# Kernel optimization log

Measured on AMD Instinct MI355X. Metric: run time of the kernel, lower is better.

The kernel has to match this reference:

```python
import jax, jax.numpy as jnp
import numpy as np

N_NODE = 100_000
N_EDGE = 2_000_000
IN_DIM = 64
OUT_DIM = 64
ATTN_DIM = 32
N_REL = 200   # rela_embed has 2*N_REL+1 = 401 rows
N_ENT = 50_000
BATCH = 8


def setup_inputs() -> dict:
    key = jax.random.key(0)
    ks = jax.random.split(key, 16)
    # edges columns: 0=r_idx (query index in batch), 2=rel, 4=sub, 5=obj; cols 1,3 unused
    r_idx = jax.random.randint(ks[0], (N_EDGE,), 0, BATCH, dtype=jnp.int32)
    rel = jax.random.randint(ks[1], (N_EDGE,), 0, 2 * N_REL + 1, dtype=jnp.int32)
    sub = jax.random.randint(ks[2], (N_EDGE,), 0, N_NODE, dtype=jnp.int32)
    obj = jax.random.randint(ks[3], (N_EDGE,), 0, N_NODE, dtype=jnp.int32)
    pad = jnp.zeros((N_EDGE,), jnp.int32)
    edges = jnp.stack([r_idx, pad, rel, pad, sub, obj], axis=1)
    nodes = jnp.stack(
        [jax.random.randint(ks[4], (N_NODE,), 0, BATCH, dtype=jnp.int32),
         jax.random.randint(ks[5], (N_NODE,), 0, N_ENT, dtype=jnp.int32)], axis=1)
    s = 0.05
    return {
        "q_sub": jax.random.randint(ks[6], (BATCH,), 0, N_ENT, dtype=jnp.int32),
        "q_rel": jax.random.randint(ks[7], (BATCH,), 0, 2 * N_REL + 1, dtype=jnp.int32),
        "hidden": jax.random.normal(ks[8], (N_NODE, IN_DIM), jnp.float32),
        "edges": edges,
        "nodes": nodes,
        "old_nodes_new_idx": jnp.arange(N_NODE // 2, dtype=jnp.int32),
        "batchsize": BATCH,
        "rela_embed": jax.random.normal(ks[9], (2 * N_REL + 1, IN_DIM), jnp.float32) * s,
        "Ws": jax.random.normal(ks[10], (ATTN_DIM, IN_DIM), jnp.float32) * s,
        "Wr": jax.random.normal(ks[11], (ATTN_DIM, IN_DIM), jnp.float32) * s,
        "Wqr": jax.random.normal(ks[12], (ATTN_DIM, IN_DIM), jnp.float32) * s,
        "bqr": jax.random.normal(ks[13], (ATTN_DIM,), jnp.float32) * s,
        "w_alpha_w": jax.random.normal(ks[14], (1, ATTN_DIM), jnp.float32) * s,
        "w_alpha_b": jnp.zeros((1,), jnp.float32),
        "Wh": jax.random.normal(ks[15], (OUT_DIM, IN_DIM), jnp.float32) * s,
    }


def reference(q_sub, q_rel, hidden, edges, nodes, old_nodes_new_idx, batchsize,
              rela_embed, Ws, Wr, Wqr, bqr, w_alpha_w, w_alpha_b, Wh):
    sub = edges[:, 4]
    rel = edges[:, 2]
    obj = edges[:, 5]
    r_idx = edges[:, 0]
    n_node = hidden.shape[0]

    hs = hidden[sub]                      # [E, in_dim] gather
    hr = rela_embed[rel]                  # [E, in_dim] gather
    h_qr = rela_embed[q_rel][r_idx]       # [E, in_dim] gather of per-query rel embed

    # attention: sigmoid(w_alpha(relu(Ws hs + Wr hr + Wqr h_qr + bqr)))
    attn = jax.nn.relu(hs @ Ws.T + hr @ Wr.T + h_qr @ Wqr.T + bqr)  # [E, attn_dim]
    alpha = jax.nn.sigmoid(attn @ w_alpha_w.T + w_alpha_b)           # [E, 1]

    message = alpha * (hs + hr)           # [E, in_dim]
    message_agg = jax.ops.segment_sum(message, obj, num_segments=n_node)  # [n_node, in_dim]
    hidden_new = message_agg @ Wh.T       # act is identity (default)
    return hidden_new
```

## Files before the change

kernel.cpp:

```cpp
#include <hip/hip_runtime.h>
#include <hip/hip_bf16.h>
#include <hip/hip_fp16.h>


typedef __attribute__((ext_vector_type(8))) short bf16x8;
typedef __attribute__((ext_vector_type(4))) float f32x4;
typedef __attribute__((ext_vector_type(2))) float f32x2;

__device__ inline unsigned short f2bf(float x) {
    unsigned u = __float_as_uint(x);
    u += 0x7FFF + ((u >> 16) & 1);
    return (unsigned short)(u >> 16);
}
__device__ inline float bf2f(unsigned short b) {
    return __uint_as_float(((unsigned)b) << 16);
}
__device__ inline __half2 u2h2(unsigned u) {
    return __builtin_bit_cast(__half2, u);
}

__device__ inline bf16x8 pack8(float4 a, float4 b) {
    bf16x8 r;
    r[0] = (short)f2bf(a.x); r[1] = (short)f2bf(a.y);
    r[2] = (short)f2bf(a.z); r[3] = (short)f2bf(a.w);
    r[4] = (short)f2bf(b.x); r[5] = (short)f2bf(b.y);
    r[6] = (short)f2bf(b.z); r[7] = (short)f2bf(b.w);
    return r;
}

template<int NT, bool F16>
__global__ void proj_mfma2_kernel(const float* __restrict__ X1, int n1,
                                  const float* __restrict__ X2, int n2,
                                  const float* __restrict__ W,
                                  unsigned short* __restrict__ out1,
                                  unsigned short* __restrict__ out2) {
    int nb1 = (n1 + 63) / 64;
    const float* X; unsigned short* out; int nrows, mblk;
    if ((int)blockIdx.x < nb1) { X = X1; out = out1; nrows = n1; mblk = blockIdx.x; }
    else                        { X = X2; out = out2; nrows = n2; mblk = blockIdx.x - nb1; }

    int lane = threadIdx.x & 63;
    int wv   = threadIdx.x >> 6;
    int m0   = (mblk * 4 + wv) * 16;
    if (m0 >= nrows) return;
    int lr = lane & 15;
    int lk = lane >> 4;

    bf16x8 bfr[NT][2];
#pragma unroll
    for (int nt = 0; nt < NT; ++nt)
#pragma unroll
        for (int ks = 0; ks < 2; ++ks) {
            const float* wp = W + (size_t)(nt * 16 + lr) * 64 + ks * 32 + lk * 8;
            float4 w0 = *(const float4*)wp;
            float4 w1 = *(const float4*)(wp + 4);
            bfr[nt][ks] = pack8(w0, w1);
        }

    int row = m0 + lr;
    if (row >= nrows) row = nrows - 1;
    const float* xp = X + (size_t)row * 64 + lk * 8;
    float4 x0 = *(const float4*)xp;
    float4 x1 = *(const float4*)(xp + 4);
    float4 x2 = *(const float4*)(xp + 32);
    float4 x3 = *(const float4*)(xp + 36);
    bf16x8 a0 = pack8(x0, x1);
    bf16x8 a1 = pack8(x2, x3);

    f32x4 acc[NT];
#pragma unroll
    for (int nt = 0; nt < NT; ++nt) {
        acc[nt] = (f32x4){0.f, 0.f, 0.f, 0.f};
        acc[nt] = __builtin_amdgcn_mfma_f32_16x16x32_bf16(a0, bfr[nt][0], acc[nt], 0, 0, 0);
        acc[nt] = __builtin_amdgcn_mfma_f32_16x16x32_bf16(a1, bfr[nt][1], acc[nt], 0, 0, 0);
    }

#pragma unroll
    for (int nt = 0; nt < NT; ++nt)
#pragma unroll
        for (int r = 0; r < 4; ++r) {
            int ro = m0 + lk * 4 + r;
            if (ro < nrows) {
                unsigned short bits;
                if (F16) {
                    __half h = __float2half(acc[nt][r]);
                    bits = __builtin_bit_cast(unsigned short, h);
                } else {
                    bits = f2bf(acc[nt][r]);
                }
                out[(size_t)ro * (NT * 16) + nt * 16 + lr] = bits;
            }
        }
}

__global__ void qproj_bf16_kernel(const int* __restrict__ q_rel, const float* __restrict__ rela,
                                  const float* __restrict__ Wqr, const float* __restrict__ bqr,
                                  unsigned* __restrict__ Qb, int batch) {
    int tid = threadIdx.x;
    int b = tid >> 5, k = tid & 31;
    if (b >= batch) return;
    int qr = q_rel[b];
    const float* x = rela + (size_t)qr * 64;
    const float* w = Wqr + (size_t)k * 64;
    float acc = bqr[k];
    for (int d = 0; d < 64; ++d) acc += w[d] * x[d];
    float other = __shfl_xor(acc, 1, 64);
    if ((k & 1) == 0) {
        unsigned lo = f2bf(acc), hi = f2bf(other);
        Qb[b * 16 + (k >> 1)] = lo | (hi << 16);
    }
}

__global__ void pack_hist_kernel(const int4* __restrict__ edges4, int2* __restrict__ pk2,
                                 int* __restrict__ hmat, int n_edge, int NB) {
    __shared__ int hist[512];
    int tid = threadIdx.x, blk = blockIdx.x;
    hist[tid] = 0;
    hist[tid + 256] = 0;
    __syncthreads();
    int unit0 = blk * 2048;
#pragma unroll
    for (int k = 0; k < 8; ++k) {
        int u = unit0 + k * 256 + tid;
        int base = u * 4;
        if (base >= n_edge) break;
        if (base + 4 <= n_edge) {
            const int4* p = edges4 + (size_t)u * 6;
            int4 v0 = p[0], v1 = p[1], v2 = p[2], v3 = p[3], v4 = p[4], v5 = p[5];
            atomicAdd(&hist[v1.y >> 8], 1);
            atomicAdd(&hist[v2.w >> 8], 1);
            atomicAdd(&hist[v4.y >> 8], 1);
            atomicAdd(&hist[v5.w >> 8], 1);
            int4 o0, o1;
            o0.x = v1.x | (v0.z << 17) | (v0.x << 26); o0.y = v1.y;
            o0.z = v2.z | (v2.x << 17) | (v1.z << 26); o0.w = v2.w;
            o1.x = v4.x | (v3.z << 17) | (v3.x << 26); o1.y = v4.y;
            o1.z = v5.z | (v5.x << 17) | (v4.z << 26); o1.w = v5.w;
            int4* q = (int4*)pk2 + (size_t)u * 2;
            q[0] = o0;
            q[1] = o1;
        } else {
            const int* ei = (const int*)edges4;
            for (int e = base; e < n_edge; ++e) {
                const int* ep = ei + (size_t)e * 6;
                int ridx = ep[0], rel = ep[2], sub = ep[4], obj = ep[5];
                atomicAdd(&hist[obj >> 8], 1);
                pk2[e] = make_int2(sub | (rel << 17) | (ridx << 26), obj);
            }
        }
    }
    __syncthreads();
    hmat[tid * NB + blk] = hist[tid];
    hmat[(tid + 256) * NB + blk] = hist[tid + 256];
}

#define SCAN_CHUNK 1024

__global__ void scan_partial_kernel(const int* __restrict__ counts, int* __restrict__ bsum,
                                    int N) {
    __shared__ int s[256];
    int base = blockIdx.x * SCAN_CHUNK;
    int tid = threadIdx.x;
    int sum = 0;
#pragma unroll
    for (int k = 0; k < 4; ++k) {
        int idx = base + k * 256 + tid;
        if (idx < N) sum += counts[idx];
    }
    s[tid] = sum;
    __syncthreads();
    for (int off = 128; off > 0; off >>= 1) {
        if (tid < off) s[tid] += s[tid + off];
        __syncthreads();
    }
    if (tid == 0) bsum[blockIdx.x] = s[0];
}

__global__ void scan_bsum_kernel(int* __restrict__ bsum, int* __restrict__ offs, int B, int N) {
    __shared__ int s[1024];
    int tid = threadIdx.x;
    int v = (tid < B) ? bsum[tid] : 0;
    s[tid] = v;
    __syncthreads();
    for (int off = 1; off < 1024; off <<= 1) {
        int t = (tid >= off) ? s[tid - off] : 0;
        __syncthreads();
        s[tid] += t;
        __syncthreads();
    }
    if (tid < B) bsum[tid] = s[tid] - v;
    if (tid == 0) offs[N] = s[1023];
}

__global__ void scan_final_kernel(const int* __restrict__ counts, const int* __restrict__ bsum,
                                  int* __restrict__ offs, int N) {
    __shared__ int s[256];
    int base = blockIdx.x * SCAN_CHUNK;
    int tid = threadIdx.x;
    int v[4];
    int sum = 0;
#pragma unroll
    for (int k = 0; k < 4; ++k) {
        int idx = base + tid * 4 + k;
        v[k] = (idx < N) ? counts[idx] : 0;
        sum += v[k];
    }
    s[tid] = sum;
    __syncthreads();
    for (int off = 1; off < 256; off <<= 1) {
        int t = (tid >= off) ? s[tid - off] : 0;
        __syncthreads();
        s[tid] += t;
        __syncthreads();
    }
    int run = bsum[blockIdx.x] + s[tid] - sum;
#pragma unroll
    for (int k = 0; k < 4; ++k) {
        int idx = base + tid * 4 + k;
        if (idx < N) offs[idx] = run;
        run += v[k];
    }
}

__global__ void scatter1_kernel(const int2* __restrict__ pk2, const int* __restrict__ hscan,
                                int2* __restrict__ outrec, int n_edge, int NB) {
    __shared__ int cur[512];
    int tid = threadIdx.x, blk = blockIdx.x;
    cur[tid] = hscan[tid * NB + blk];
    cur[tid + 256] = hscan[(tid + 256) * NB + blk];
    __syncthreads();
    int unit0 = blk * 2048;
#pragma unroll
    for (int k = 0; k < 8; ++k) {
        int u = unit0 + k * 256 + tid;
        int base = u * 4;
        if (base >= n_edge) break;
        if (base + 4 <= n_edge) {
            const int4* q = (const int4*)pk2 + (size_t)u * 2;
            int4 a = q[0], b = q[1];
            int p0 = atomicAdd(&cur[(a.y >> 8) & 0x1FF], 1);
            int p1 = atomicAdd(&cur[(a.w >> 8) & 0x1FF], 1);
            int p2 = atomicAdd(&cur[(b.y >> 8) & 0x1FF], 1);
            int p3 = atomicAdd(&cur[(b.w >> 8) & 0x1FF], 1);
            outrec[p0] = make_int2(a.x, a.y);
            outrec[p1] = make_int2(a.z, a.w);
            outrec[p2] = make_int2(b.x, b.y);
            outrec[p3] = make_int2(b.z, b.w);
        } else {
            for (int e = base; e < n_edge; ++e) {
                int2 r = pk2[e];
                int p = atomicAdd(&cur[(r.y >> 8) & 0x1FF], 1);
                outrec[p] = r;
            }
        }
    }
}

#define BS_CAP 8192
__global__ __launch_bounds__(512) void bucket_sort_kernel(const int2* __restrict__ in,
                                                          const int* __restrict__ hscan,
                                                          int* __restrict__ hdrS,
                                                          int* __restrict__ offs,
                                                          int NB, int n_node) {
    __shared__ int hist[256];
    __shared__ int sbase[256];
    __shared__ int cur[256];
    __shared__ int2 st[BS_CAP];
    int b = blockIdx.x, tid = threadIdx.x;
    int start = hscan[b * NB];
    int end   = hscan[(b + 1) * NB];
    int size  = end - start;
    if (tid < 256) hist[tid] = 0;
    __syncthreads();
    bool inlds = (size <= BS_CAP);
    if (inlds) {
        for (int i = tid; i < size; i += 512) {
            int2 v = in[start + i];
            st[i] = v;
            atomicAdd(&hist[v.y & 255], 1);
        }
    } else {
        for (int i = tid; i < size; i += 512) {
            int2 v = in[start + i];
            atomicAdd(&hist[v.y & 255], 1);
        }
    }
    __syncthreads();
    int h = 0;
    if (tid < 256) { h = hist[tid]; sbase[tid] = h; }
    __syncthreads();
    for (int off = 1; off < 256; off <<= 1) {
        int t = (tid >= off && tid < 256) ? sbase[tid - off] : 0;
        __syncthreads();
        if (tid < 256) sbase[tid] += t;
        __syncthreads();
    }
    if (tid < 256) {
        int ebase = sbase[tid] - h;
        cur[tid] = ebase;
        int obj = (b << 8) | tid;
        if (obj <= n_node) offs[obj] = start + ebase;
    }
    __syncthreads();
    if (inlds) {
        for (int i = tid; i < size; i += 512) {
            int2 r = st[i];
            int p = atomicAdd(&cur[r.y & 255], 1);
            hdrS[start + p] = r.x;
        }
    } else {
        for (int i = tid; i < size; i += 512) {
            int2 r = in[start + i];
            int p = atomicAdd(&cur[r.y & 255], 1);
            hdrS[start + p] = r.x;
        }
    }
}

__device__ inline float edot(unsigned sv, unsigned rv, unsigned qv, float2 w) {
    float a0 = fmaxf(bf2f((unsigned short)sv) + bf2f((unsigned short)rv)
                     + bf2f((unsigned short)qv), 0.f);
    float a1 = fmaxf(bf2f((unsigned short)(sv >> 16)) + bf2f((unsigned short)(rv >> 16))
                     + bf2f((unsigned short)(qv >> 16)), 0.f);
    return a0 * w.x + a1 * w.y;
}

__global__ void alpha_kernel(const int* __restrict__ hdrS,
                             const unsigned* __restrict__ Sb,
                             const unsigned* __restrict__ Rb,
                             const unsigned* __restrict__ Qb,
                             const float2* __restrict__ w2,
                             const float* __restrict__ w_alpha_b,
                             float* __restrict__ af,
                             int n_edge) {
    int tid = threadIdx.x;
    int lane = tid & 15;
    int e0 = (blockIdx.x * 16 + (tid >> 4)) * 4;
    if (e0 >= n_edge) return;
    int4 h4 = *(const int4*)(hdrS + e0);
    int h0 = h4.x, h1 = h4.y, h2 = h4.z, h3 = h4.w;
    float2 w = w2[lane];
    unsigned sv0 = Sb[(size_t)(h0 & 0x1FFFF) * 16 + lane];
    unsigned sv1 = Sb[(size_t)(h1 & 0x1FFFF) * 16 + lane];
    unsigned sv2 = Sb[(size_t)(h2 & 0x1FFFF) * 16 + lane];
    unsigned sv3 = Sb[(size_t)(h3 & 0x1FFFF) * 16 + lane];
    unsigned rv0 = Rb[(size_t)((h0 >> 17) & 0x1FF) * 16 + lane];
    unsigned rv1 = Rb[(size_t)((h1 >> 17) & 0x1FF) * 16 + lane];
    unsigned rv2 = Rb[(size_t)((h2 >> 17) & 0x1FF) * 16 + lane];
    unsigned rv3 = Rb[(size_t)((h3 >> 17) & 0x1FF) * 16 + lane];
    unsigned qv0 = Qb[((h0 >> 26) & 7) * 16 + lane];
    unsigned qv1 = Qb[((h1 >> 26) & 7) * 16 + lane];
    unsigned qv2 = Qb[((h2 >> 26) & 7) * 16 + lane];
    unsigned qv3 = Qb[((h3 >> 26) & 7) * 16 + lane];
    float p0 = edot(sv0, rv0, qv0, w);
    float p1 = edot(sv1, rv1, qv1, w);
    float p2 = edot(sv2, rv2, qv2, w);
    float p3 = edot(sv3, rv3, qv3, w);
#pragma unroll
    for (int off = 8; off > 0; off >>= 1) {
        p0 += __shfl_xor(p0, off, 16);
        p1 += __shfl_xor(p1, off, 16);
        p2 += __shfl_xor(p2, off, 16);
        p3 += __shfl_xor(p3, off, 16);
    }
    if (lane < 4 && e0 + lane < n_edge) {
        float p = p0;
        if (lane == 1) p = p1;
        if (lane == 2) p = p2;
        if (lane == 3) p = p3;
        float alpha = 1.f / (1.f + __expf(-(p + w_alpha_b[0])));
        af[e0 + lane] = alpha;
    }
}

__global__ void reduce_kernel(const int* __restrict__ hdrS, const float* __restrict__ af,
                              const int* __restrict__ offs,
                              const uint2* __restrict__ Hw2,
                              const uint2* __restrict__ Rw2,
                              float4* __restrict__ out4, int n_node) {
    int lane = threadIdx.x & 63;
    int node = blockIdx.x * 4 + (threadIdx.x >> 6);
    if (node >= n_node) return;
    int g = lane >> 4;
    int t = lane & 15;
    int start = offs[node], end = offs[node + 1];
    __half2 acc0 = __float2half2_rn(0.f);
    __half2 acc1 = __float2half2_rn(0.f);

    for (int i = start; i < end; i += 64) {
        int m = end - i;
        if (m > 64) m = 64;
        float a = 0.f;
        int pk = 0;
        if (lane < m) {
            a  = __builtin_nontemporal_load(&af[i + lane]);
            pk = __builtin_nontemporal_load(&hdrS[i + lane]);
        }
        int nj = (m + 3) >> 2;

        __half2 A0, A1, A2, A3;
        uint2 H0, H1, H2, H3, R0, R1, R2, R3;

#define RD_ISSUE(S, J) do {                                                   \
        int src_ = 4 * (J) + g;                                               \
        bool ok_ = (src_ < m);                                                \
        int s_ = ok_ ? src_ : 0;                                              \
        float a_ = __shfl(a, s_, 64);                                         \
        int p_ = __shfl(pk, s_, 64);                                          \
        A##S = __float2half2_rn(ok_ ? a_ : 0.f);                              \
        int sub_ = p_ & 0x1FFFF, rel_ = (p_ >> 17) & 0x1FF;                   \
        H##S = Hw2[(size_t)sub_ * 16 + t];                                    \
        R##S = Rw2[(size_t)rel_ * 16 + t];                                    \
    } while (0)

#define RD_CONSUME(S) do {                                                    \
        acc0 = __hfma2(A##S, __hadd2(u2h2(H##S.x), u2h2(R##S.x)), acc0);      \
        acc1 = __hfma2(A##S, __hadd2(u2h2(H##S.y), u2h2(R##S.y)), acc1);      \
    } while (0)

        RD_ISSUE(0, 0);
        RD_ISSUE(1, 1);
        RD_ISSUE(2, 2);
        RD_ISSUE(3, 3);
        for (int j = 0; j < nj; j += 4) {
            RD_CONSUME(0); RD_ISSUE(0, j + 4);
            RD_CONSUME(1); RD_ISSUE(1, j + 5);
            RD_CONSUME(2); RD_ISSUE(2, j + 6);
            RD_CONSUME(3); RD_ISSUE(3, j + 7);
        }
#undef RD_ISSUE
#undef RD_CONSUME
    }
    float2 f0 = __half22float2(acc0);
    float2 f1 = __half22float2(acc1);
    f32x4 acc = (f32x4){f0.x, f0.y, f1.x, f1.y};
#pragma unroll
    for (int off = 16; off <= 32; off <<= 1) {
        acc.x += __shfl_xor(acc.x, off, 64);
        acc.y += __shfl_xor(acc.y, off, 64);
        acc.z += __shfl_xor(acc.z, off, 64);
        acc.w += __shfl_xor(acc.w, off, 64);
    }
    if (g == 0)
        __builtin_nontemporal_store(acc, (f32x4*)&out4[(size_t)node * 16 + t]);
}

extern "C" void kernel_launch(void* const* d_in, const int* in_sizes, int n_in,
                              void* d_out, int out_size, void* d_ws, size_t ws_size,
                              hipStream_t stream) {
    const int*   q_rel     = (const int*)d_in[1];
    const float* hidden    = (const float*)d_in[2];
    const int*   edges     = (const int*)d_in[3];
    const float* rela      = (const float*)d_in[7];
    const float* Ws        = (const float*)d_in[8];
    const float* Wr        = (const float*)d_in[9];
    const float* Wqr       = (const float*)d_in[10];
    const float* bqr       = (const float*)d_in[11];
    const float* w_alpha_w = (const float*)d_in[12];
    const float* w_alpha_b = (const float*)d_in[13];
    const float* Wh        = (const float*)d_in[14];

    int n_node = in_sizes[2] / 64;
    int n_edge = in_sizes[3] / 6;
    int n_rel  = in_sizes[7] / 64;
    int batch  = in_sizes[1];

    int NB = (n_edge + 8191) / 8192;
    int N2 = NB * 512;
    int n_sblk2 = (N2 + SCAN_CHUNK - 1) / SCAN_CHUNK;

    unsigned* Sb   = (unsigned*)d_ws;
    unsigned* Rb   = Sb + (size_t)n_node * 16;
    unsigned* Qb   = Rb + (size_t)n_rel * 16;
    int*   offs    = (int*)(Qb + (size_t)batch * 16);
    int*   bsum    = offs + n_node + 1;
    int*   hmat    = bsum + 1024;
    int*   hscan   = hmat + N2;
    size_t rec_off = (size_t)(hscan + N2 + 1 - (int*)d_ws);
    rec_off = (rec_off + 3) & ~(size_t)3;
    int2*  regP    = (int2*)((int*)d_ws + rec_off);
    int2*  regQ    = regP + n_edge;
    int*   hdrS    = (int*)regP;
    float* af      = (float*)(hdrS + n_edge);
    unsigned short* Hw = (unsigned short*)regQ;
    unsigned short* Rw = Hw + (size_t)n_node * 64;

    {
        int nb = (n_node + 63) / 64 + (n_rel + 63) / 64;
        proj_mfma2_kernel<2, false><<<nb, 256, 0, stream>>>(
            hidden, n_node, rela, n_rel, Ws, (unsigned short*)Sb, (unsigned short*)Rb);
    }
    qproj_bf16_kernel<<<1, 256, 0, stream>>>(q_rel, rela, Wqr, bqr, Qb, batch);

    pack_hist_kernel<<<NB, 256, 0, stream>>>((const int4*)edges, regP, hmat, n_edge, NB);

    scan_partial_kernel<<<n_sblk2, 256, 0, stream>>>(hmat, bsum, N2);
    scan_bsum_kernel<<<1, 1024, 0, stream>>>(bsum, hscan, n_sblk2, N2);
    scan_final_kernel<<<n_sblk2, 256, 0, stream>>>(hmat, bsum, hscan, N2);

    scatter1_kernel<<<NB, 256, 0, stream>>>(regP, hscan, regQ, n_edge, NB);
    bucket_sort_kernel<<<512, 512, 0, stream>>>(regQ, hscan, hdrS, offs, NB, n_node);

    alpha_kernel<<<(n_edge + 63) / 64, 256, 0, stream>>>(
        hdrS, Sb, Rb, Qb, (const float2*)w_alpha_w, w_alpha_b, af, n_edge);

    {
        int nb = (n_node + 63) / 64 + (n_rel + 63) / 64;
        proj_mfma2_kernel<4, true><<<nb, 256, 0, stream>>>(
            hidden, n_node, rela, n_rel, Wh, Hw, Rw);
    }

    reduce_kernel<<<(n_node + 3) / 4, 256, 0, stream>>>(
        hdrS, af, offs, (const uint2*)Hw, (const uint2*)Rw, (float4*)d_out, n_node);
}
```

Measured before the change: 304.1 us.

## Stage radix scatter through LDS to coalesce bucket writes

The first-pass radix scatter now loads each block's 8192 records, builds a local histogram, and scans it. It then sorts the records by bucket in shared memory before writing them out. Writes to global memory become contiguous runs per bucket instead of random 8-byte stores. The cost is 64KB+ of LDS per block, which lowers occupancy, plus extra syncs and a 512-step scan per block.

```diff
diff --git a/kernel.cpp b/kernel.cpp
--- a/kernel.cpp
+++ b/kernel.cpp
@@ -222,37 +222,58 @@
     }
 }
 
-__global__ void scatter1_kernel(const int2* __restrict__ pk2, const int* __restrict__ hscan,
-                                int2* __restrict__ outrec, int n_edge, int NB) {
-    __shared__ int cur[512];
+__global__ __launch_bounds__(512) void scatter1_kernel(const int2* __restrict__ pk2,
+                                                       const int* __restrict__ hscan,
+                                                       int2* __restrict__ outrec,
+                                                       int n_edge, int NB) {
+    __shared__ int lhist[512];
+    __shared__ int lincl[512];
+    __shared__ int lcur[512];
+    __shared__ int gbase[512];
+    __shared__ int2 st[8192];
     int tid = threadIdx.x, blk = blockIdx.x;
-    cur[tid] = hscan[tid * NB + blk];
-    cur[tid + 256] = hscan[(tid + 256) * NB + blk];
-    __syncthreads();
-    int unit0 = blk * 2048;
-#pragma unroll
-    for (int k = 0; k < 8; ++k) {
-        int u = unit0 + k * 256 + tid;
-        int base = u * 4;
-        if (base >= n_edge) break;
-        if (base + 4 <= n_edge) {
-            const int4* q = (const int4*)pk2 + (size_t)u * 2;
-            int4 a = q[0], b = q[1];
-            int p0 = atomicAdd(&cur[(a.y >> 8) & 0x1FF], 1);
-            int p1 = atomicAdd(&cur[(a.w >> 8) & 0x1FF], 1);
-            int p2 = atomicAdd(&cur[(b.y >> 8) & 0x1FF], 1);
-            int p3 = atomicAdd(&cur[(b.w >> 8) & 0x1FF], 1);
-            outrec[p0] = make_int2(a.x, a.y);
-            outrec[p1] = make_int2(a.z, a.w);
-            outrec[p2] = make_int2(b.x, b.y);
-            outrec[p3] = make_int2(b.z, b.w);
-        } else {
-            for (int e = base; e < n_edge; ++e) {
-                int2 r = pk2[e];
-                int p = atomicAdd(&cur[(r.y >> 8) & 0x1FF], 1);
-                outrec[p] = r;
-            }
-        }
+    int start_e = blk * 8192;
+    int cnt = n_edge - start_e;
+    if (cnt > 8192) cnt = 8192;
+    lhist[tid] = 0;
+    gbase[tid] = hscan[tid * NB + blk];
+    __syncthreads();
+    int2 r[16];
+#pragma unroll
+    for (int k = 0; k < 16; ++k) {
+        int idx = tid + k * 512;
+        if (idx < cnt) {
+            r[k] = pk2[start_e + idx];
+            atomicAdd(&lhist[(r[k].y >> 8) & 511], 1);
+        }
+    }
+    __syncthreads();
+    int h = lhist[tid];
+    lincl[tid] = h;
+    __syncthreads();
+    for (int off = 1; off < 512; off <<= 1) {
+        int t = (tid >= off) ? lincl[tid - off] : 0;
+        __syncthreads();
+        lincl[tid] += t;
+        __syncthreads();
+    }
+    lcur[tid] = lincl[tid] - h;
+    __syncthreads();
+#pragma unroll
+    for (int k = 0; k < 16; ++k) {
+        int idx = tid + k * 512;
+        if (idx < cnt) {
+            int b = (r[k].y >> 8) & 511;
+            int p = atomicAdd(&lcur[b], 1);
+            st[p] = r[k];
+        }
+    }
+    __syncthreads();
+    for (int i = tid; i < cnt; i += 512) {
+        int2 rec = st[i];
+        int b = (rec.y >> 8) & 511;
+        int lrank = i - (lincl[b] - lhist[b]);
+        outrec[gbase[b] + lrank] = rec;
     }
 }
 
@@ -498,7 +519,7 @@
     scan_bsum_kernel<<<1, 1024, 0, stream>>>(bsum, hscan, n_sblk2, N2);
     scan_final_kernel<<<n_sblk2, 256, 0, stream>>>(hmat, bsum, hscan, N2);
 
-    scatter1_kernel<<<NB, 256, 0, stream>>>(regP, hscan, regQ, n_edge, NB);
+    scatter1_kernel<<<NB, 512, 0, stream>>>(regP, hscan, regQ, n_edge, NB);
     bucket_sort_kernel<<<512, 512, 0, stream>>>(regQ, hscan, hdrS, offs, NB, n_node);
 
     alpha_kernel<<<(n_edge + 63) / 64, 256, 0, stream>>>(
```

Result: no change. 303.2 us (-0.3%).
